# Performance work log

Measured on AMD Instinct MI355X. Metric: run time of the kernel, lower is better.

Reference implementation:

```python
import jax, jax.numpy as jnp
import numpy as np

ENTITY_TYPES = ['PER', 'ORG', 'LOC', 'MISC', 'GPE', 'DATE', 'TIME', 'MONEY', 'PERCENT',
                'FAC', 'EVENT', 'LAW', 'LANGUAGE', 'NORP', 'ORDINAL', 'CARDINAL', 'PRODUCT', 'QUANTITY']
TAGS = ['<PAD>', 'O'] + [f'{p}-{t}' for t in ENTITY_TYPES for p in ('B', 'I')]
TAG2IDX = {t: i for i, t in enumerate(TAGS)}
PAD_IDX = TAG2IDX['<PAD>']
O_IDX = TAG2IDX['O']
LAMBDA_MISS = 1.2
LAMBDA_FP = 1.0
LAMBDA_TRANSITION = 0.8
EPS = 1e-8


def _split_tag(tag):
    if tag in {'O', '<PAD>'} or '-' not in tag:
        return (tag, None)
    prefix, label = tag.split('-', 1)
    return (prefix, label)


def build_valid_transition_mask():
    n = len(TAGS)
    valid = np.zeros((n, n), dtype=np.float32)
    for prev_idx, prev_tag in enumerate(TAGS):
        prev_prefix, prev_label = _split_tag(prev_tag)
        for curr_idx, curr_tag in enumerate(TAGS):
            curr_prefix, curr_label = _split_tag(curr_tag)
            if curr_tag == '<PAD>' or curr_tag == 'O' or curr_prefix == 'B':
                ok = True
            elif curr_prefix == 'I':
                ok = (prev_prefix in {'B', 'I'}) and (prev_label == curr_label)
            else:
                ok = False
            valid[prev_idx, curr_idx] = 1.0 if ok else 0.0
    return valid


def setup_inputs() -> dict:
    key = jax.random.key(0)
    k1, k2 = jax.random.split(key)
    B, T, C = 128, 4096, len(TAGS)  # C = 38
    logits = jax.random.normal(k1, (B, T, C), dtype=jnp.float32)
    labels = jax.random.randint(k2, (B, T), 0, C, dtype=jnp.int32)
    valid_transition_mask = jnp.asarray(build_valid_transition_mask())  # [C, C]
    return {'logits': logits, 'labels': labels, 'valid_transition_mask': valid_transition_mask}


def _masked_mean(x, mask):
    # mean of x over positions where mask is True (0 if mask empty)
    cnt = jnp.sum(mask)
    return jnp.sum(jnp.where(mask, x, 0.0)) / jnp.maximum(cnt, 1).astype(x.dtype)


def reference(logits, labels, valid_transition_mask):
    # logits: [B, T, C]; labels: [B, T] int; valid_transition_mask: [C, C]
    logp = jax.nn.log_softmax(logits, axis=-1)            # [B, T, C]
    probs = jnp.exp(logp)                                  # softmax(logits)

    valid = labels != PAD_IDX                              # [B, T]
    # cross entropy with ignore_index=PAD (unweighted mean over valid tokens)
    gold_logp = jnp.take_along_axis(logp, labels[..., None], axis=-1)[..., 0]
    ce_loss = _masked_mean(-gold_logp, valid)

    p_o = probs[..., O_IDX]                                # [B, T]
    gold_entity = valid & (labels != O_IDX)
    gold_o = valid & (labels == O_IDX)

    # miss penalty: -log(1 - p_o) on gold entity tokens
    miss_penalty = _masked_mean(-jnp.log(jnp.clip(1.0 - p_o, EPS)), gold_entity)
    # false-positive penalty: -log(1 - (1 - p_o)) = -log(p_o) on gold O tokens
    fp_penalty = _masked_mean(-jnp.log(jnp.clip(p_o, EPS)), gold_o)

    # transition penalty: sum of prev_probs (outer) curr_probs over invalid (prev,curr)
    # pairs. Algebraically: prev . (invalid @ curr) per position, avoids [B,T,C,C].
    invalid = 1.0 - valid_transition_mask                  # [C, C]
    invalid_mass = jnp.einsum('btc,cd,btd->bt', probs[:, :-1, :], invalid, probs[:, 1:, :])
    tmask = valid[:, 1:] & valid[:, :-1]
    transition_penalty = _masked_mean(invalid_mass, tmask)

    return (ce_loss + LAMBDA_MISS * miss_penalty + LAMBDA_FP * fp_penalty
            + LAMBDA_TRANSITION * transition_penalty)
```

## Files before the change

kernel.cpp:

```cpp
#include <hip/hip_runtime.h>


#define NCLS 38
#define ROWMASK 4095


template<int OFF>
__device__ __forceinline__ void softmax_tok(float (&v)[76], int lab,
                                            float& mx, float& s, float& gold) {
    mx = v[OFF];
#pragma unroll
    for (int c = 1; c < NCLS; ++c) mx = fmaxf(mx, v[OFF + c]);
    gold = v[OFF];
#pragma unroll
    for (int c = 1; c < NCLS; ++c) if (lab == c) gold = v[OFF + c];
    s = 0.f;
#pragma unroll
    for (int c = 0; c < NCLS; ++c) {
        float e = __expf(v[OFF + c] - mx);
        v[OFF + c] = e;
        s += e;
    }
}

__global__ __launch_bounds__(256) void ner_main(const float* __restrict__ logits,
                                                const int* __restrict__ labels,
                                                float* __restrict__ ws) {
    __shared__ float eq[257][19];
    __shared__ float red[4][8];

    const int tid = threadIdx.x;
    const long long a = (long long)blockIdx.x * 512 + 2 * tid;

    float v[76];
    const float4* src = reinterpret_cast<const float4*>(logits + a * NCLS);
#pragma unroll
    for (int i = 0; i < 19; ++i) reinterpret_cast<float4*>(v)[i] = src[i];

    const int2 lab2 = *reinterpret_cast<const int2*>(labels + a);
    const int la = lab2.x, lb = lab2.y;

    float mxa, sa, golda, mxb, sb, goldb;
    softmax_tok<0>(v, la, mxa, sa, golda);
    softmax_tok<38>(v, lb, mxb, sb, goldb);
    const float inva = 1.f / sa, invb = 1.f / sb;
    const float logsa = __logf(sa), logsb = __logf(sb);
#pragma unroll
    for (int c = 0; c < 76; ++c) v[c] *= (c < 38 ? inva : invb);
    const float spa = sa * inva;
    const float spb = sb * invb;

    float ce_s = 0.f, miss_s = 0.f, fp_s = 0.f, tr_s = 0.f;
    float ce_c = 0.f, miss_c = 0.f, fp_c = 0.f, tr_c = 0.f;

    if (la != 0) {
        ce_s += mxa + logsa - golda; ce_c += 1.f;
        const float po = v[1];
        if (la == 1) { fp_s   -= __logf(fmaxf(po,       1e-8f)); fp_c   += 1.f; }
        else         { miss_s -= __logf(fmaxf(1.f - po, 1e-8f)); miss_c += 1.f; }
    }
    if (lb != 0) {
        ce_s += mxb + logsb - goldb; ce_c += 1.f;
        const float po = v[38 + 1];
        if (lb == 1) { fp_s   -= __logf(fmaxf(po,       1e-8f)); fp_c   += 1.f; }
        else         { miss_s -= __logf(fmaxf(1.f - po, 1e-8f)); miss_c += 1.f; }
    }

    if (la != 0 && lb != 0) {
        float m = 0.f;
#pragma unroll
        for (int j = 0; j < 18; ++j)
            m += v[38 + 3 + 2 * j] * (spa - v[2 + 2 * j] - v[3 + 2 * j]);
        tr_s += 0.f + m; tr_c += 1.f;
    }

#pragma unroll
    for (int j = 0; j < 18; ++j) eq[tid][j] = v[3 + 2 * j];

    const bool rowend = ((a + 1) & ROWMASK) == ROWMASK;
    if (tid == 255 && !rowend) {
        float w[38];
        const float* p2 = logits + (a + 2) * NCLS;
        const float4* s2 = reinterpret_cast<const float4*>(p2);
#pragma unroll
        for (int i = 0; i < 9; ++i) reinterpret_cast<float4*>(w)[i] = s2[i];
        reinterpret_cast<float2*>(w)[18] = reinterpret_cast<const float2*>(p2)[18];
        float mx = w[0];
#pragma unroll
        for (int c = 1; c < NCLS; ++c) mx = fmaxf(mx, w[c]);
        float s = 0.f;
#pragma unroll
        for (int c = 0; c < NCLS; ++c) { float e = __expf(w[c] - mx); w[c] = e; s += e; }
        const float inv = 1.f / s;
#pragma unroll
        for (int j = 0; j < 18; ++j) eq[256][j] = w[3 + 2 * j] * inv;
    }
    __syncthreads();

    if (!rowend) {
        const int lnext = labels[a + 2];
        if (lb != 0 && lnext != 0) {
            float m = 0.f;
#pragma unroll
            for (int j = 0; j < 18; ++j)
                m += eq[tid + 1][j] * (spb - v[38 + 2 + 2 * j] - v[38 + 3 + 2 * j]);
            tr_s += m; tr_c += 1.f;
        }
    }

    float vals[8] = {ce_s, miss_s, fp_s, tr_s, ce_c, miss_c, fp_c, tr_c};
#pragma unroll
    for (int k = 0; k < 8; ++k) {
        float x = vals[k];
#pragma unroll
        for (int off = 32; off >= 1; off >>= 1) x += __shfl_down(x, off, 64);
        vals[k] = x;
    }
    const int lane = tid & 63, wv = tid >> 6;
    if (lane == 0) {
#pragma unroll
        for (int k = 0; k < 8; ++k) red[wv][k] = vals[k];
    }
    __syncthreads();
    if (tid < 8) {
        const float t = red[0][tid] + red[1][tid] + red[2][tid] + red[3][tid];
        atomicAdd(ws + tid * 16, t);
    }
}

__global__ void ner_finalize(const float* __restrict__ ws, float* __restrict__ out) {
    if (threadIdx.x == 0) {
        const float ce = ws[0 * 16] / fmaxf(ws[4 * 16], 1.f);
        const float mi = ws[1 * 16] / fmaxf(ws[5 * 16], 1.f);
        const float fp = ws[2 * 16] / fmaxf(ws[6 * 16], 1.f);
        const float tr = ws[3 * 16] / fmaxf(ws[7 * 16], 1.f);
        out[0] = ce + 1.2f * mi + 1.0f * fp + 0.8f * tr;
    }
}

extern "C" void kernel_launch(void* const* d_in, const int* in_sizes, int n_in,
                              void* d_out, int out_size, void* d_ws, size_t ws_size,
                              hipStream_t stream) {
    const float* logits = (const float*)d_in[0];
    const int*   labels = (const int*)d_in[1];
    float* ws = (float*)d_ws;

    const long long N = (long long)in_sizes[1];
    const int blocks = (int)(N / 512);

    hipMemsetAsync(d_ws, 0, 128 * sizeof(float), stream);
    hipLaunchKernelGGL(ner_main, dim3(blocks), dim3(256), 0, stream, logits, labels, ws);
    hipLaunchKernelGGL(ner_finalize, dim3(1), dim3(64), 0, stream, ws, (float*)d_out);
}
```

Before: 134.2 us.

## Stage logits through LDS with coalesced loads, one token per thread

```diff
diff --git a/kernel.cpp b/kernel.cpp
--- a/kernel.cpp
+++ b/kernel.cpp
@@ -2,113 +2,98 @@
 
 
 #define NCLS 38
+#define TPB 256
 #define ROWMASK 4095
 
 
-template<int OFF>
-__device__ __forceinline__ void softmax_tok(float (&v)[76], int lab,
-                                            float& mx, float& s, float& gold) {
-    mx = v[OFF];
-#pragma unroll
-    for (int c = 1; c < NCLS; ++c) mx = fmaxf(mx, v[OFF + c]);
-    gold = v[OFF];
-#pragma unroll
-    for (int c = 1; c < NCLS; ++c) if (lab == c) gold = v[OFF + c];
-    s = 0.f;
-#pragma unroll
-    for (int c = 0; c < NCLS; ++c) {
-        float e = __expf(v[OFF + c] - mx);
-        v[OFF + c] = e;
-        s += e;
-    }
-}
-
-__global__ __launch_bounds__(256) void ner_main(const float* __restrict__ logits,
-                                                const int* __restrict__ labels,
-                                                float* __restrict__ ws) {
-    __shared__ float eq[257][19];
+__global__ __launch_bounds__(256, 4) void ner_main(const float* __restrict__ logits,
+                                                   const int* __restrict__ labels,
+                                                   float* __restrict__ ws,
+                                                   int nblocks) {
+    __shared__ float lds[TPB * NCLS + NCLS];
     __shared__ float red[4][8];
 
     const int tid = threadIdx.x;
-    const long long a = (long long)blockIdx.x * 512 + 2 * tid;
+    const int b   = blockIdx.x;
+    const long long tok = (long long)b * TPB + tid;
 
-    float v[76];
-    const float4* src = reinterpret_cast<const float4*>(logits + a * NCLS);
+    {
+        const float4* g4 = reinterpret_cast<const float4*>(logits + (long long)b * TPB * NCLS);
+        float4* l4 = reinterpret_cast<float4*>(lds);
 #pragma unroll
-    for (int i = 0; i < 19; ++i) reinterpret_cast<float4*>(v)[i] = src[i];
+        for (int i = 0; i < 10; ++i) {
+            const int idx = tid + i * TPB;
+            if (idx < TPB * NCLS / 4) l4[idx] = g4[idx];
+        }
+        if (b + 1 < nblocks && tid < NCLS)
+            lds[TPB * NCLS + tid] = logits[(long long)(b + 1) * TPB * NCLS + tid];
+    }
+    __syncthreads();
 
-    const int2 lab2 = *reinterpret_cast<const int2*>(labels + a);
-    const int la = lab2.x, lb = lab2.y;
+    const int l = labels[tok];
 
-    float mxa, sa, golda, mxb, sb, goldb;
-    softmax_tok<0>(v, la, mxa, sa, golda);
-    softmax_tok<38>(v, lb, mxb, sb, goldb);
-    const float inva = 1.f / sa, invb = 1.f / sb;
-    const float logsa = __logf(sa), logsb = __logf(sb);
+    float v[NCLS];
+    {
+        float2* vv = reinterpret_cast<float2*>(v);
+        const float2* lp = reinterpret_cast<const float2*>(lds + tid * NCLS);
 #pragma unroll
-    for (int c = 0; c < 76; ++c) v[c] *= (c < 38 ? inva : invb);
-    const float spa = sa * inva;
-    const float spb = sb * invb;
+        for (int i = 0; i < NCLS / 2; ++i) vv[i] = lp[i];
+    }
+    const float gold = lds[tid * NCLS + l];
 
-    float ce_s = 0.f, miss_s = 0.f, fp_s = 0.f, tr_s = 0.f;
-    float ce_c = 0.f, miss_c = 0.f, fp_c = 0.f, tr_c = 0.f;
+    float mx = v[0];
+#pragma unroll
+    for (int c = 1; c < NCLS; ++c) mx = fmaxf(mx, v[c]);
+    float s = 0.f;
+#pragma unroll
+    for (int c = 0; c < NCLS; ++c) { const float e = __expf(v[c] - mx); v[c] = e; s += e; }
+    const float inv = 1.f / s;
+#pragma unroll
+    for (int c = 0; c < NCLS; ++c) v[c] *= inv;
+    const float sp = s * inv;
+    const float lg = __logf(s);
 
-    if (la != 0) {
-        ce_s += mxa + logsa - golda; ce_c += 1.f;
+    float ce_s = 0.f, mi_s = 0.f, fp_s = 0.f, tr_s = 0.f;
+    float ce_c = 0.f, mi_c = 0.f, fp_c = 0.f, tr_c = 0.f;
+
+    if (l != 0) {
+        ce_s = mx + lg - gold; ce_c = 1.f;
         const float po = v[1];
-        if (la == 1) { fp_s   -= __logf(fmaxf(po,       1e-8f)); fp_c   += 1.f; }
-        else         { miss_s -= __logf(fmaxf(1.f - po, 1e-8f)); miss_c += 1.f; }
-    }
-    if (lb != 0) {
-        ce_s += mxb + logsb - goldb; ce_c += 1.f;
-        const float po = v[38 + 1];
-        if (lb == 1) { fp_s   -= __logf(fmaxf(po,       1e-8f)); fp_c   += 1.f; }
-        else         { miss_s -= __logf(fmaxf(1.f - po, 1e-8f)); miss_c += 1.f; }
-    }
-
-    if (la != 0 && lb != 0) {
-        float m = 0.f;
-#pragma unroll
-        for (int j = 0; j < 18; ++j)
-            m += v[38 + 3 + 2 * j] * (spa - v[2 + 2 * j] - v[3 + 2 * j]);
-        tr_s += 0.f + m; tr_c += 1.f;
+        if (l == 1) { fp_s = -__logf(fmaxf(po,       1e-8f)); fp_c = 1.f; }
+        else        { mi_s = -__logf(fmaxf(1.f - po, 1e-8f)); mi_c = 1.f; }
     }
 
 #pragma unroll
-    for (int j = 0; j < 18; ++j) eq[tid][j] = v[3 + 2 * j];
-
-    const bool rowend = ((a + 1) & ROWMASK) == ROWMASK;
-    if (tid == 255 && !rowend) {
-        float w[38];
-        const float* p2 = logits + (a + 2) * NCLS;
-        const float4* s2 = reinterpret_cast<const float4*>(p2);
-#pragma unroll
-        for (int i = 0; i < 9; ++i) reinterpret_cast<float4*>(w)[i] = s2[i];
-        reinterpret_cast<float2*>(w)[18] = reinterpret_cast<const float2*>(p2)[18];
-        float mx = w[0];
-#pragma unroll
-        for (int c = 1; c < NCLS; ++c) mx = fmaxf(mx, w[c]);
-        float s = 0.f;
-#pragma unroll
-        for (int c = 0; c < NCLS; ++c) { float e = __expf(w[c] - mx); w[c] = e; s += e; }
-        const float inv = 1.f / s;
-#pragma unroll
-        for (int j = 0; j < 18; ++j) eq[256][j] = w[3 + 2 * j] * inv;
-    }
+    for (int j = 0; j < 18; ++j) lds[tid * NCLS + j] = v[3 + 2 * j];
     __syncthreads();
 
-    if (!rowend) {
-        const int lnext = labels[a + 2];
-        if (lb != 0 && lnext != 0) {
+    const bool rowend = ((tok & ROWMASK) == ROWMASK);
+    if (!rowend && l != 0) {
+        const int lnext = labels[tok + 1];
+        if (lnext != 0) {
             float m = 0.f;
+            if (tid < TPB - 1) {
 #pragma unroll
-            for (int j = 0; j < 18; ++j)
-                m += eq[tid + 1][j] * (spb - v[38 + 2 + 2 * j] - v[38 + 3 + 2 * j]);
-            tr_s += m; tr_c += 1.f;
+                for (int j = 0; j < 18; ++j)
+                    m += lds[(tid + 1) * NCLS + j] * (sp - v[2 + 2 * j] - v[3 + 2 * j]);
+            } else {
+                const float* g = lds + TPB * NCLS;
+                float bmx = g[0];
+#pragma unroll
+                for (int c = 1; c < NCLS; ++c) bmx = fmaxf(bmx, g[c]);
+                float bs = 0.f;
+#pragma unroll
+                for (int c = 0; c < NCLS; ++c) bs += __expf(g[c] - bmx);
+                const float binv = 1.f / bs;
+#pragma unroll
+                for (int j = 0; j < 18; ++j)
+                    m += __expf(g[3 + 2 * j] - bmx) * binv * (sp - v[2 + 2 * j] - v[3 + 2 * j]);
+            }
+            tr_s = m; tr_c = 1.f;
         }
     }
 
-    float vals[8] = {ce_s, miss_s, fp_s, tr_s, ce_c, miss_c, fp_c, tr_c};
+    float vals[8] = {ce_s, mi_s, fp_s, tr_s, ce_c, mi_c, fp_c, tr_c};
 #pragma unroll
     for (int k = 0; k < 8; ++k) {
         float x = vals[k];
@@ -146,9 +131,9 @@
     float* ws = (float*)d_ws;
 
     const long long N = (long long)in_sizes[1];
-    const int blocks = (int)(N / 512);
+    const int blocks = (int)(N / TPB);
 
     hipMemsetAsync(d_ws, 0, 128 * sizeof(float), stream);
-    hipLaunchKernelGGL(ner_main, dim3(blocks), dim3(256), 0, stream, logits, labels, ws);
+    hipLaunchKernelGGL(ner_main, dim3(blocks), dim3(TPB), 0, stream, logits, labels, ws, blocks);
     hipLaunchKernelGGL(ner_finalize, dim3(1), dim3(64), 0, stream, ws, (float*)d_out);
 }
```

After: 154.7 us. 1.15x slower.
